# Performance work log

Measured on AMD Instinct MI355X. Metric: run time of the kernel, lower is better.

## Reference

```python
import jax, jax.numpy as jnp
import numpy as np

NUM_HEADS = 16

def setup_inputs() -> dict:
    key = jax.random.key(0)
    ks = jax.random.split(key, 5)
    d_model = 1024
    x = jax.random.normal(ks[0], (2, 2048, d_model), dtype=jnp.float32)
    # xavier-uniform-like scale for square [d_model, d_model] weights
    lim = float(np.sqrt(6.0 / (d_model + d_model)))
    def w(k):
        return jax.random.uniform(k, (d_model, d_model), dtype=jnp.float32, minval=-lim, maxval=lim)
    return {"x": x, "Wq": w(ks[1]), "Wk": w(ks[2]), "Wv": w(ks[3]), "Wo": w(ks[4])}

def reference(x, Wq, Wk, Wv, Wo):
    B, S, D = x.shape
    H = NUM_HEADS
    dk = D // H
    # project: torch does x @ W.T
    def split_heads(t):
        return t.reshape(B, S, H, dk).transpose(0, 2, 1, 3)  # [B,H,S,dk]
    q = split_heads(x @ Wq.T)
    k = split_heads(x @ Wk.T)
    v = split_heads(x @ Wv.T)
    scores = jnp.einsum('bhqd,bhkd->bhqk', q, k) / jnp.sqrt(jnp.float32(dk))
    causal = jnp.tril(jnp.ones((S, S), dtype=bool))  # True where attended
    scores = jnp.where(causal[None, None], scores, -jnp.inf)
    probs = jax.nn.softmax(scores, axis=-1)
    out = jnp.einsum('bhqk,bhkd->bhqd', probs, v)  # [B,H,S,dk]
    out = out.transpose(0, 2, 1, 3).reshape(B, S, D)
    return out @ Wo.T
```

## Files before the change

kernel.cpp:

```cpp
#include <hip/hip_runtime.h>
#include <stdint.h>

#define BATCH  2
#define SEQ    2048
#define DMODEL 1024
#define NHEADS 16
#define DKH    64
#define MTOT   (BATCH*SEQ)
#define VSTR   (SEQ + 32)

typedef unsigned short u16;
typedef __bf16 bf16x8 __attribute__((ext_vector_type(8)));
typedef float  f32x4  __attribute__((ext_vector_type(4)));

extern "C" __device__ float __ocml_native_exp2_f32(float);

__device__ __forceinline__ u16 f2bf(float f) {
  union { float f; uint32_t u; } v; v.f = f;
  uint32_t u = v.u;
  return (u16)((u + 0x7FFFu + ((u >> 16) & 1u)) >> 16);
}
__device__ __forceinline__ float bf2f(u16 h) {
  union { uint32_t u; float f; } v; v.u = (uint32_t)h << 16; return v.f;
}

__device__ __forceinline__ void gld_lds16(const void* g, void* l) {
  __builtin_amdgcn_global_load_lds(
      (__attribute__((address_space(1))) void*)g,
      (__attribute__((address_space(3))) void*)l, 16, 0, 0);
}

__global__ void cvt_f32_bf16(const float* __restrict__ src, u16* __restrict__ dst) {
  size_t i = ((size_t)blockIdx.x * 256 + threadIdx.x) * 4;
  float4 f = *(const float4*)(src + i);
  ushort4 o;
  o.x = f2bf(f.x); o.y = f2bf(f.y); o.z = f2bf(f.z); o.w = f2bf(f.w);
  *(ushort4*)(dst + i) = o;
}
__global__ void cvt_w(const float* __restrict__ a, const float* __restrict__ b,
                      const float* __restrict__ c, const float* __restrict__ d,
                      u16* __restrict__ dst) {
  const float* srcs[4] = {a, b, c, d};
  const float* s = srcs[blockIdx.y];
  size_t i = ((size_t)blockIdx.x * 256 + threadIdx.x) * 4;
  float4 f = *(const float4*)(s + i);
  ushort4 o;
  o.x = f2bf(f.x); o.y = f2bf(f.y); o.z = f2bf(f.z); o.w = f2bf(f.w);
  *(ushort4*)(dst + (size_t)blockIdx.y * (DMODEL*DMODEL) + i) = o;
}

__device__ __forceinline__ void gemm_core64(const u16* A, const u16* W,
                                            int m0, int n0, f32x4 acc[4][2],
                                            u16* lA, u16* lB) {
  const int tid  = threadIdx.x;
  const int lane = tid & 63;
  const int lrow = lane & 15;
  const int quad = lane >> 4;
  const int wave = tid >> 6;
  const int wm   = (wave & 1) * 64;
  const int wn   = (wave >> 1) * 32;
  const int sx   = lrow & 7;

  for (int k0 = 0; k0 < DMODEL; k0 += 64) {
    #pragma unroll
    for (int r = 0; r < 4; ++r) {
      int off  = r * 4096 + tid * 16;
      int row  = off >> 7;
      int c16  = (off >> 4) & 7;
      int colb = (c16 ^ (row & 7)) << 4;
      gld_lds16((const char*)A + ((size_t)(m0 + row) * DMODEL + k0) * 2 + colb,
                (char*)lA + off);
    }
    #pragma unroll
    for (int r = 0; r < 2; ++r) {
      int off  = r * 4096 + tid * 16;
      int row  = off >> 7;
      int c16  = (off >> 4) & 7;
      int colb = (c16 ^ (row & 7)) << 4;
      gld_lds16((const char*)W + ((size_t)(n0 + row) * DMODEL + k0) * 2 + colb,
                (char*)lB + off);
    }
    __syncthreads();
    #pragma unroll
    for (int ks = 0; ks < 2; ++ks) {
      bf16x8 a[4], b[2];
      const int ro = ((((ks << 2) | quad) ^ sx) << 3);
      #pragma unroll
      for (int i = 0; i < 4; ++i)
        a[i] = *(const bf16x8*)(lA + (wm + i*16 + lrow) * 64 + ro);
      #pragma unroll
      for (int j = 0; j < 2; ++j)
        b[j] = *(const bf16x8*)(lB + (wn + j*16 + lrow) * 64 + ro);
      #pragma unroll
      for (int i = 0; i < 4; ++i)
        #pragma unroll
        for (int j = 0; j < 2; ++j)
          acc[i][j] = __builtin_amdgcn_mfma_f32_16x16x32_bf16(a[i], b[j], acc[i][j], 0, 0, 0);
    }
    __syncthreads();
  }
}

__global__ __launch_bounds__(256, 3) void gemm_qkv(
    const u16* __restrict__ xb, const u16* __restrict__ wq,
    const u16* __restrict__ wk, const u16* __restrict__ wv,
    u16* __restrict__ q, u16* __restrict__ k, u16* __restrict__ v, float qscale) {
  __shared__ __align__(16) u16 lA[128 * 64];
  __shared__ __align__(16) u16 lB[64 * 64];
  const int z = blockIdx.z;
  const u16* W = (z == 0) ? wq : (z == 1) ? wk : wv;
  u16* out     = (z == 0) ? q  : (z == 1) ? k  : v;
  const float scale = (z == 0) ? qscale : 1.0f;
  const int m0 = blockIdx.x * 128, n0 = blockIdx.y * 64;
  f32x4 acc[4][2] = {};
  gemm_core64(xb, W, m0, n0, acc, lA, lB);

  const int lane = threadIdx.x & 63;
  const int wave = threadIdx.x >> 6;
  const int wm = (wave & 1) * 64, wn = (wave >> 1) * 32;
  const int rb = (lane >> 4) * 4, cb = lane & 15;
  const int h = n0 >> 6;
  if (z == 2) {
    #pragma unroll
    for (int i = 0; i < 4; ++i)
      #pragma unroll
      for (int j = 0; j < 2; ++j) {
        int row0 = m0 + wm + i*16 + rb;
        int d_   = wn + j*16 + cb;
        int b_ = row0 >> 11, s0 = row0 & 2047;
        ushort4 pk;
        pk.x = f2bf(acc[i][j][0]); pk.y = f2bf(acc[i][j][1]);
        pk.z = f2bf(acc[i][j][2]); pk.w = f2bf(acc[i][j][3]);
        *(ushort4*)&out[((size_t)(b_*NHEADS + h) * DKH + d_) * VSTR + s0] = pk;
      }
  } else {
    #pragma unroll
    for (int i = 0; i < 4; ++i)
      #pragma unroll
      for (int j = 0; j < 2; ++j)
        #pragma unroll
        for (int r = 0; r < 4; ++r) {
          int row = m0 + wm + i*16 + rb + r;
          int d_  = wn + j*16 + cb;
          int b_ = row >> 11, s_ = row & 2047;
          out[(((size_t)(b_*NHEADS + h) * SEQ + s_) << 6) + d_] =
              f2bf(acc[i][j][r] * scale);
        }
  }
}

__global__ __launch_bounds__(256, 3) void gemm_out(
    const u16* __restrict__ ab, const u16* __restrict__ wo, float* __restrict__ out) {
  __shared__ __align__(16) u16 lA[128 * 64];
  __shared__ __align__(16) u16 lB[64 * 64];
  const int m0 = blockIdx.x * 128, n0 = blockIdx.y * 64;
  f32x4 acc[4][2] = {};
  gemm_core64(ab, wo, m0, n0, acc, lA, lB);

  const int lane = threadIdx.x & 63;
  const int wave = threadIdx.x >> 6;
  const int wm = (wave & 1) * 64, wn = (wave >> 1) * 32;
  const int rb = (lane >> 4) * 4, cb = lane & 15;
  #pragma unroll
  for (int i = 0; i < 4; ++i)
    #pragma unroll
    for (int j = 0; j < 2; ++j)
      #pragma unroll
      for (int r = 0; r < 4; ++r)
        out[(size_t)(m0 + wm + i*16 + rb + r) * DMODEL + (n0 + wn + j*16 + cb)]
            = acc[i][j][r];
}

#define PSTR 68
__device__ const uint8_t JT[60] = {
  124,125,120,121,116,117,112,113,108,109,104,105,100,101,96,97,92,93,
  88,84,80,76,72,68,64,60,56,52,48,44,
  89,40, 85,36, 81,32, 126,77,28, 122,73,24, 118,69,20, 114,65,16,
  110,61,12, 106,57,8, 102,53,4, 98,49,0
};

__global__ __launch_bounds__(64, 2) void attn(
    const u16* __restrict__ Q, const u16* __restrict__ K,
    const u16* __restrict__ V, u16* __restrict__ O,
    u16* __restrict__ po, float* __restrict__ pl) {
  __shared__ __align__(16) u16 Ps[4][16 * PSTR];

  const int lane = threadIdx.x & 63;
  const int lrow = lane & 15;
  const int quad = lane >> 4;
  const int kq   = quad * 8;

  const int g  = blockIdx.x >> 5;
  const int bh = blockIdx.x & 31;
  const int e  = JT[g];
  const int p  = e >> 2, c = e & 3;
  const int lo = c * 12;
  const int hi = (p + 1 < lo + 12) ? p + 1 : lo + 12;

  const u16* Qg = Q + (size_t)bh * SEQ * DKH;
  const u16* Kg = K + (size_t)bh * SEQ * DKH;
  const u16* Vg = V + (size_t)bh * DKH * VSTR;

  bf16x8 aq[4][2];
  #pragma unroll
  for (int i = 0; i < 4; ++i)
    #pragma unroll
    for (int ks = 0; ks < 2; ++ks)
      aq[i][ks] = *(const bf16x8*)(Qg + (size_t)(64*p + 16*i + lrow) * DKH + ks*32 + kq);

  f32x4 o_acc[4][4] = {};
  float l_acc[4][4] = {};

  const u16* kbase = Kg + (size_t)lrow * DKH + kq;
  const u16* vbase = Vg + (size_t)lrow * VSTR + kq;

  for (int t = lo; t < hi; ++t) {
    bf16x8 kf[2][4], vf[2][4];
    #pragma unroll
    for (int ks = 0; ks < 2; ++ks)
      #pragma unroll
      for (int j = 0; j < 4; ++j) {
        kf[ks][j] = *(const bf16x8*)(kbase + (size_t)t*64*DKH + j*16*DKH + ks*32);
        vf[ks][j] = *(const bf16x8*)(vbase + t*64 + (size_t)j*16*VSTR + ks*32);
      }
    const bool mk = (t == p);

    #pragma unroll
    for (int i = 0; i < 4; ++i) {
      f32x4 s_acc[4] = {};
      #pragma unroll
      for (int ks = 0; ks < 2; ++ks)
        #pragma unroll
        for (int j = 0; j < 4; ++j)
          s_acc[j] = __builtin_amdgcn_mfma_f32_16x16x32_bf16(aq[i][ks], kf[ks][j], s_acc[j], 0, 0, 0);

      if (mk) {
        const int qloc = 16*i + quad*4;
        #pragma unroll
        for (int j = 0; j < 4; ++j) {
          int kloc = j*16 + lrow;
          #pragma unroll
          for (int r = 0; r < 4; ++r)
            if (kloc > qloc + r) s_acc[j][r] = -1e30f;
        }
      }

      #pragma unroll
      for (int j = 0; j < 4; ++j)
        #pragma unroll
        for (int r = 0; r < 4; ++r) {
          float pv = __ocml_native_exp2_f32(s_acc[j][r]);
          l_acc[i][r] += pv;
          union { float f; uint32_t u; } cv; cv.f = pv;
          Ps[i][(quad*4 + r) * PSTR + j*16 + lrow] = (u16)(cv.u >> 16);
        }

      #pragma unroll
      for (int ks = 0; ks < 2; ++ks) {
        bf16x8 ap = *(const bf16x8*)(&Ps[i][lrow * PSTR + ks*32 + kq]);
        #pragma unroll
        for (int j = 0; j < 4; ++j)
          o_acc[i][j] = __builtin_amdgcn_mfma_f32_16x16x32_bf16(ap, vf[ks][j], o_acc[i][j], 0, 0, 0);
      }
    }
  }

  float lr[4][4];
  #pragma unroll
  for (int i = 0; i < 4; ++i)
    #pragma unroll
    for (int r = 0; r < 4; ++r) {
      float sm = l_acc[i][r];
      #pragma unroll
      for (int d = 1; d < 16; d <<= 1) sm += __shfl_xor(sm, d, 64);
      lr[i][r] = sm;
    }

  if (p <= 11) {
    const int h = bh & 15, b_ = bh >> 4;
    #pragma unroll
    for (int i = 0; i < 4; ++i)
      #pragma unroll
      for (int j = 0; j < 4; ++j)
        #pragma unroll
        for (int r = 0; r < 4; ++r) {
          int sg = 64*p + 16*i + quad*4 + r;
          O[(size_t)(b_ * SEQ + sg) * DMODEL + h * DKH + j*16 + lrow]
              = f2bf(o_acc[i][j][r] / lr[i][r]);
        }
  } else {
    const int base = (p < 24) ? (p - 12) * 2 : 24 + (p - 24) * 3;
    const int slot = (base + c) * 32 + bh;
    #pragma unroll
    for (int i = 0; i < 4; ++i) {
      #pragma unroll
      for (int j = 0; j < 4; ++j) {
        ushort4 pk;
        pk.x = f2bf(o_acc[i][j][0]); pk.y = f2bf(o_acc[i][j][1]);
        pk.z = f2bf(o_acc[i][j][2]); pk.w = f2bf(o_acc[i][j][3]);
        *(ushort4*)&po[(size_t)slot * 4096 + (j*16 + lrow) * 64 + 16*i + quad*4] = pk;
      }
      if (lrow == 0)
        #pragma unroll
        for (int r = 0; r < 4; ++r)
          pl[slot * 64 + 16*i + quad*4 + r] = lr[i][r];
    }
  }
}

__global__ __launch_bounds__(256) void combine(
    const u16* __restrict__ po, const float* __restrict__ pl, u16* __restrict__ ab) {
  __shared__ u16 Ls[64][68];
  const int b  = blockIdx.x;
  const int p  = 12 + (b >> 5);
  const int bh = b & 31;
  const int t  = threadIdx.x;
  const int col = t >> 2;
  const int r0  = (t & 3) * 16;
  const int base = (p < 24) ? (p - 12) * 2 : 24 + (p - 24) * 3;
  const int nc   = (p < 24) ? 2 : 3;

  float acc[16], lsum[16];
  {
    const size_t s0 = (size_t)(base * 32 + bh);
    const u16*   q0 = po + s0 * 4096 + col * 64 + r0;
    const float* l0 = pl + s0 * 64 + r0;
    #pragma unroll
    for (int q4 = 0; q4 < 4; ++q4) {
      ushort4 a = *(const ushort4*)(q0 + q4 * 4);
      ushort4 c2 = *(const ushort4*)(q0 + 32 * 4096 + q4 * 4);
      acc[q4*4+0] = bf2f(a.x) + bf2f(c2.x);
      acc[q4*4+1] = bf2f(a.y) + bf2f(c2.y);
      acc[q4*4+2] = bf2f(a.z) + bf2f(c2.z);
      acc[q4*4+3] = bf2f(a.w) + bf2f(c2.w);
      float4 f = *(const float4*)(l0 + q4 * 4);
      float4 g = *(const float4*)(l0 + 32 * 64 + q4 * 4);
      lsum[q4*4+0] = f.x + g.x; lsum[q4*4+1] = f.y + g.y;
      lsum[q4*4+2] = f.z + g.z; lsum[q4*4+3] = f.w + g.w;
    }
    if (nc == 3) {
      const u16*   q2 = q0 + (size_t)64 * 4096;
      const float* l2 = l0 + (size_t)64 * 64;
      #pragma unroll
      for (int q4 = 0; q4 < 4; ++q4) {
        ushort4 a = *(const ushort4*)(q2 + q4 * 4);
        acc[q4*4+0] += bf2f(a.x); acc[q4*4+1] += bf2f(a.y);
        acc[q4*4+2] += bf2f(a.z); acc[q4*4+3] += bf2f(a.w);
        float4 f = *(const float4*)(l2 + q4 * 4);
        lsum[q4*4+0] += f.x; lsum[q4*4+1] += f.y;
        lsum[q4*4+2] += f.z; lsum[q4*4+3] += f.w;
      }
    }
  }
  #pragma unroll
  for (int q = 0; q < 16; ++q)
    Ls[r0 + q][col] = f2bf(acc[q] / lsum[q]);
  __syncthreads();

  const int row = t >> 2;
  const int c0  = (t & 3) * 16;
  const int b_ = bh >> 4, h = bh & 15;
  u16* dst = ab + (size_t)(b_ * SEQ + 64 * p + row) * DMODEL + h * DKH + c0;
  #pragma unroll
  for (int q = 0; q < 16; q += 4)
    *(ushort4*)(dst + q) = *(const ushort4*)&Ls[row][c0 + q];
}

extern "C" void kernel_launch(void* const* d_in, const int* in_sizes, int n_in,
                              void* d_out, int out_size, void* d_ws, size_t ws_size,
                              hipStream_t stream) {
  const float* x  = (const float*)d_in[0];
  const float* Wq = (const float*)d_in[1];
  const float* Wk = (const float*)d_in[2];
  const float* Wv = (const float*)d_in[3];
  const float* Wo = (const float*)d_in[4];
  float* out = (float*)d_out;

  u16* xb  = (u16*)d_ws;
  u16* wqb = xb  + (size_t)MTOT * DMODEL;
  u16* wkb = wqb + (size_t)DMODEL * DMODEL;
  u16* wvb = wkb + (size_t)DMODEL * DMODEL;
  u16* wob = wvb + (size_t)DMODEL * DMODEL;
  u16* qb  = wob + (size_t)DMODEL * DMODEL;
  u16* kb  = qb  + (size_t)MTOT * DMODEL;
  u16* vb  = kb  + (size_t)MTOT * DMODEL;
  u16* ab  = vb  + (size_t)BATCH * NHEADS * DKH * VSTR;
  u16* po  = xb;
  float* pl = (float*)(po + (size_t)1536 * 4096);

  cvt_f32_bf16<<<MTOT * DMODEL / 1024, 256, 0, stream>>>(x, xb);
  cvt_w<<<dim3(DMODEL * DMODEL / 1024, 4), 256, 0, stream>>>(Wq, Wk, Wv, Wo, wqb);

  const float qscale = 0.125f * 1.44269504088896340736f;
  gemm_qkv<<<dim3(32, 16, 3), 256, 0, stream>>>(
      xb, wqb, wkb, wvb, qb, kb, vb, qscale);

  attn<<<1920, 64, 0, stream>>>(qb, kb, vb, ab, po, pl);
  combine<<<640, 256, 0, stream>>>(po, pl, ab);

  gemm_out<<<dim3(32, 16), 256, 0, stream>>>(ab, wob, out);
}
```

Measured before the change: 176.2 us.

## Fuse QKV projections into one GEMM tile and split attention KV into finer chunks

The QKV GEMM now computes Q, K and V for the same 128x64 tile in one block, loading each x tile into LDS once and reusing it across three weight tiles, instead of launching three separate z-slices. This cuts repeated reads of x and launches a third as many blocks, but each block holds three times the accumulators and more LDS, which may lower occupancy. The causal attention split also changes from 12-block to 8-block KV chunks, giving more work items (2560) and a reworked combine for up to four partials, to balance load better. The partial buffers are moved to a separate workspace region because they no longer fit in the reused xb area.

After: 171.3 us. -2.8%, faster.

```diff
diff --git a/kernel.cpp b/kernel.cpp
--- a/kernel.cpp
+++ b/kernel.cpp
@@ -47,6 +47,108 @@
   ushort4 o;
   o.x = f2bf(f.x); o.y = f2bf(f.y); o.z = f2bf(f.z); o.w = f2bf(f.w);
   *(ushort4*)(dst + (size_t)blockIdx.y * (DMODEL*DMODEL) + i) = o;
+}
+
+__global__ __launch_bounds__(256, 3) void gemm_qkv(
+    const u16* __restrict__ xb, const u16* __restrict__ wq,
+    const u16* __restrict__ wk, const u16* __restrict__ wv,
+    u16* __restrict__ q, u16* __restrict__ k, u16* __restrict__ v, float qscale) {
+  __shared__ __align__(16) u16 lA[128 * 64];
+  __shared__ __align__(16) u16 lB[3][64 * 64];
+
+  const int tid  = threadIdx.x;
+  const int lane = tid & 63;
+  const int lrow = lane & 15;
+  const int quad = lane >> 4;
+  const int wave = tid >> 6;
+  const int wm   = (wave & 1) * 64;
+  const int wn   = (wave >> 1) * 32;
+  const int sx   = lrow & 7;
+  const int m0 = blockIdx.x * 128, n0 = blockIdx.y * 64;
+  const u16* Ws[3] = {wq, wk, wv};
+
+  f32x4 acc[3][4][2] = {};
+
+  for (int k0 = 0; k0 < DMODEL; k0 += 64) {
+    #pragma unroll
+    for (int r = 0; r < 4; ++r) {
+      int off  = r * 4096 + tid * 16;
+      int row  = off >> 7;
+      int c16  = (off >> 4) & 7;
+      int colb = (c16 ^ (row & 7)) << 4;
+      gld_lds16((const char*)xb + ((size_t)(m0 + row) * DMODEL + k0) * 2 + colb,
+                (char*)lA + off);
+    }
+    #pragma unroll
+    for (int z = 0; z < 3; ++z)
+      #pragma unroll
+      for (int r = 0; r < 2; ++r) {
+        int off  = r * 4096 + tid * 16;
+        int row  = off >> 7;
+        int c16  = (off >> 4) & 7;
+        int colb = (c16 ^ (row & 7)) << 4;
+        gld_lds16((const char*)Ws[z] + ((size_t)(n0 + row) * DMODEL + k0) * 2 + colb,
+                  (char*)&lB[z][0] + off);
+      }
+    __syncthreads();
+    #pragma unroll
+    for (int ks = 0; ks < 2; ++ks) {
+      const int ro = ((((ks << 2) | quad) ^ sx) << 3);
+      bf16x8 a[4], b[3][2];
+      #pragma unroll
+      for (int i = 0; i < 4; ++i)
+        a[i] = *(const bf16x8*)(lA + (wm + i*16 + lrow) * 64 + ro);
+      #pragma unroll
+      for (int z = 0; z < 3; ++z)
+        #pragma unroll
+        for (int j = 0; j < 2; ++j)
+          b[z][j] = *(const bf16x8*)(&lB[z][0] + (wn + j*16 + lrow) * 64 + ro);
+      #pragma unroll
+      for (int z = 0; z < 3; ++z)
+        #pragma unroll
+        for (int i = 0; i < 4; ++i)
+          #pragma unroll
+          for (int j = 0; j < 2; ++j)
+            acc[z][i][j] = __builtin_amdgcn_mfma_f32_16x16x32_bf16(a[i], b[z][j], acc[z][i][j], 0, 0, 0);
+    }
+    __syncthreads();
+  }
+
+  const int rb = quad * 4, cb = lrow;
+  const int h  = blockIdx.y;
+  u16* outs[3] = {q, k, v};
+  #pragma unroll
+  for (int z = 0; z < 3; ++z) {
+    u16* out = outs[z];
+    if (z == 2) {
+      #pragma unroll
+      for (int i = 0; i < 4; ++i)
+        #pragma unroll
+        for (int j = 0; j < 2; ++j) {
+          int row0 = m0 + wm + i*16 + rb;
+          int d_   = wn + j*16 + cb;
+          int b_ = row0 >> 11, s0 = row0 & 2047;
+          ushort4 pk;
+          pk.x = f2bf(acc[z][i][j][0]); pk.y = f2bf(acc[z][i][j][1]);
+          pk.z = f2bf(acc[z][i][j][2]); pk.w = f2bf(acc[z][i][j][3]);
+          *(ushort4*)&out[((size_t)(b_*NHEADS + h) * DKH + d_) * VSTR + s0] = pk;
+        }
+    } else {
+      const float scale = (z == 0) ? qscale : 1.0f;
+      #pragma unroll
+      for (int i = 0; i < 4; ++i)
+        #pragma unroll
+        for (int j = 0; j < 2; ++j)
+          #pragma unroll
+          for (int r = 0; r < 4; ++r) {
+            int row = m0 + wm + i*16 + rb + r;
+            int d_  = wn + j*16 + cb;
+            int b_ = row >> 11, s_ = row & 2047;
+            out[(((size_t)(b_*NHEADS + h) * SEQ + s_) << 6) + d_] =
+                f2bf(acc[z][i][j][r] * scale);
+          }
+    }
+  }
 }
 
 __device__ __forceinline__ void gemm_core64(const u16* A, const u16* W,
@@ -101,54 +203,6 @@
   }
 }
 
-__global__ __launch_bounds__(256, 3) void gemm_qkv(
-    const u16* __restrict__ xb, const u16* __restrict__ wq,
-    const u16* __restrict__ wk, const u16* __restrict__ wv,
-    u16* __restrict__ q, u16* __restrict__ k, u16* __restrict__ v, float qscale) {
-  __shared__ __align__(16) u16 lA[128 * 64];
-  __shared__ __align__(16) u16 lB[64 * 64];
-  const int z = blockIdx.z;
-  const u16* W = (z == 0) ? wq : (z == 1) ? wk : wv;
-  u16* out     = (z == 0) ? q  : (z == 1) ? k  : v;
-  const float scale = (z == 0) ? qscale : 1.0f;
-  const int m0 = blockIdx.x * 128, n0 = blockIdx.y * 64;
-  f32x4 acc[4][2] = {};
-  gemm_core64(xb, W, m0, n0, acc, lA, lB);
-
-  const int lane = threadIdx.x & 63;
-  const int wave = threadIdx.x >> 6;
-  const int wm = (wave & 1) * 64, wn = (wave >> 1) * 32;
-  const int rb = (lane >> 4) * 4, cb = lane & 15;
-  const int h = n0 >> 6;
-  if (z == 2) {
-    #pragma unroll
-    for (int i = 0; i < 4; ++i)
-      #pragma unroll
-      for (int j = 0; j < 2; ++j) {
-        int row0 = m0 + wm + i*16 + rb;
-        int d_   = wn + j*16 + cb;
-        int b_ = row0 >> 11, s0 = row0 & 2047;
-        ushort4 pk;
-        pk.x = f2bf(acc[i][j][0]); pk.y = f2bf(acc[i][j][1]);
-        pk.z = f2bf(acc[i][j][2]); pk.w = f2bf(acc[i][j][3]);
-        *(ushort4*)&out[((size_t)(b_*NHEADS + h) * DKH + d_) * VSTR + s0] = pk;
-      }
-  } else {
-    #pragma unroll
-    for (int i = 0; i < 4; ++i)
-      #pragma unroll
-      for (int j = 0; j < 2; ++j)
-        #pragma unroll
-        for (int r = 0; r < 4; ++r) {
-          int row = m0 + wm + i*16 + rb + r;
-          int d_  = wn + j*16 + cb;
-          int b_ = row >> 11, s_ = row & 2047;
-          out[(((size_t)(b_*NHEADS + h) * SEQ + s_) << 6) + d_] =
-              f2bf(acc[i][j][r] * scale);
-        }
-  }
-}
-
 __global__ __launch_bounds__(256, 3) void gemm_out(
     const u16* __restrict__ ab, const u16* __restrict__ wo, float* __restrict__ out) {
   __shared__ __align__(16) u16 lA[128 * 64];
@@ -172,11 +226,12 @@
 }
 
 #define PSTR 68
-__device__ const uint8_t JT[60] = {
-  124,125,120,121,116,117,112,113,108,109,104,105,100,101,96,97,92,93,
-  88,84,80,76,72,68,64,60,56,52,48,44,
-  89,40, 85,36, 81,32, 126,77,28, 122,73,24, 118,69,20, 114,65,16,
-  110,61,12, 106,57,8, 102,53,4, 98,49,0
+__device__ const uint8_t JT[80] = {
+  124,125,126,127, 120,121,122, 116,117,118, 112,113,114, 108,109,110,
+  104,105,106, 100,101,102, 96,97,98, 92,93,94, 88,89, 84,85, 80,81,
+  76,77, 72,73, 68,69, 64,65, 60,61, 56, 52, 48, 44, 40, 36, 32, 28,
+  123,90,57,24, 119,86,53,20, 115,82,49,16, 111,78,45,12,
+  107,74,41,8, 103,70,37,4, 99,66,33,0
 };
 
 __global__ __launch_bounds__(64, 2) void attn(
@@ -194,8 +249,8 @@
   const int bh = blockIdx.x & 31;
   const int e  = JT[g];
   const int p  = e >> 2, c = e & 3;
-  const int lo = c * 12;
-  const int hi = (p + 1 < lo + 12) ? p + 1 : lo + 12;
+  const int lo = c * 8;
+  const int hi = (p + 1 < lo + 8) ? p + 1 : lo + 8;
 
   const u16* Qg = Q + (size_t)bh * SEQ * DKH;
   const u16* Kg = K + (size_t)bh * SEQ * DKH;
@@ -276,7 +331,7 @@
       lr[i][r] = sm;
     }
 
-  if (p <= 11) {
+  if (p <= 7) {
     const int h = bh & 15, b_ = bh >> 4;
     #pragma unroll
     for (int i = 0; i < 4; ++i)
@@ -289,7 +344,9 @@
               = f2bf(o_acc[i][j][r] / lr[i][r]);
         }
   } else {
-    const int base = (p < 24) ? (p - 12) * 2 : 24 + (p - 24) * 3;
+    const int base = (p < 16) ? (p - 8) * 2
+                   : (p < 24) ? 16 + (p - 16) * 3
+                   :            40 + (p - 24) * 4;
     const int slot = (base + c) * 32 + bh;
     #pragma unroll
     for (int i = 0; i < 4; ++i) {
@@ -312,44 +369,53 @@
     const u16* __restrict__ po, const float* __restrict__ pl, u16* __restrict__ ab) {
   __shared__ u16 Ls[64][68];
   const int b  = blockIdx.x;
-  const int p  = 12 + (b >> 5);
+  const int p  = 8 + (b >> 5);
   const int bh = b & 31;
   const int t  = threadIdx.x;
   const int col = t >> 2;
   const int r0  = (t & 3) * 16;
-  const int base = (p < 24) ? (p - 12) * 2 : 24 + (p - 24) * 3;
-  const int nc   = (p < 24) ? 2 : 3;
+  const int base = (p < 16) ? (p - 8) * 2
+                 : (p < 24) ? 16 + (p - 16) * 3
+                 :            40 + (p - 24) * 4;
+  const int nc   = (p < 16) ? 2 : (p < 24) ? 3 : 4;
 
   float acc[16], lsum[16];
-  {
-    const size_t s0 = (size_t)(base * 32 + bh);
-    const u16*   q0 = po + s0 * 4096 + col * 64 + r0;
-    const float* l0 = pl + s0 * 64 + r0;
+  const size_t s0 = (size_t)(base * 32 + bh);
+  const u16*   q0 = po + s0 * 4096 + col * 64 + r0;
+  const float* l0 = pl + s0 * 64 + r0;
+  #pragma unroll
+  for (int q4 = 0; q4 < 4; ++q4) {
+    ushort4 a  = *(const ushort4*)(q0 + q4 * 4);
+    ushort4 c2 = *(const ushort4*)(q0 + (size_t)32 * 4096 + q4 * 4);
+    acc[q4*4+0] = bf2f(a.x) + bf2f(c2.x);
+    acc[q4*4+1] = bf2f(a.y) + bf2f(c2.y);
+    acc[q4*4+2] = bf2f(a.z) + bf2f(c2.z);
+    acc[q4*4+3] = bf2f(a.w) + bf2f(c2.w);
+    float4 f = *(const float4*)(l0 + q4 * 4);
+    float4 g = *(const float4*)(l0 + 32 * 64 + q4 * 4);
+    lsum[q4*4+0] = f.x + g.x; lsum[q4*4+1] = f.y + g.y;
+    lsum[q4*4+2] = f.z + g.z; lsum[q4*4+3] = f.w + g.w;
+  }
+  if (nc >= 3) {
     #pragma unroll
     for (int q4 = 0; q4 < 4; ++q4) {
-      ushort4 a = *(const ushort4*)(q0 + q4 * 4);
-      ushort4 c2 = *(const ushort4*)(q0 + 32 * 4096 + q4 * 4);
-      acc[q4*4+0] = bf2f(a.x) + bf2f(c2.x);
-      acc[q4*4+1] = bf2f(a.y) + bf2f(c2.y);
-      acc[q4*4+2] = bf2f(a.z) + bf2f(c2.z);
-      acc[q4*4+3] = bf2f(a.w) + bf2f(c2.w);
-      float4 f = *(const float4*)(l0 + q4 * 4);
-      float4 g = *(const float4*)(l0 + 32 * 64 + q4 * 4);
-      lsum[q4*4+0] = f.x + g.x; lsum[q4*4+1] = f.y + g.y;
-      lsum[q4*4+2] = f.z + g.z; lsum[q4*4+3] = f.w + g.w;
-    }
-    if (nc == 3) {
-      const u16*   q2 = q0 + (size_t)64 * 4096;
-      const float* l2 = l0 + (size_t)64 * 64;
-      #pragma unroll
-      for (int q4 = 0; q4 < 4; ++q4) {
-        ushort4 a = *(const ushort4*)(q2 + q4 * 4);
-        acc[q4*4+0] += bf2f(a.x); acc[q4*4+1] += bf2f(a.y);
-        acc[q4*4+2] += bf2f(a.z); acc[q4*4+3] += bf2f(a.w);
-        float4 f = *(const float4*)(l2 + q4 * 4);
-        lsum[q4*4+0] += f.x; lsum[q4*4+1] += f.y;
-        lsum[q4*4+2] += f.z; lsum[q4*4+3] += f.w;
-      }
+      ushort4 a = *(const ushort4*)(q0 + (size_t)64 * 4096 + q4 * 4);
+      acc[q4*4+0] += bf2f(a.x); acc[q4*4+1] += bf2f(a.y);
+      acc[q4*4+2] += bf2f(a.z); acc[q4*4+3] += bf2f(a.w);
+      float4 f = *(const float4*)(l0 + 64 * 64 + q4 * 4);
+      lsum[q4*4+0] += f.x; lsum[q4*4+1] += f.y;
+      lsum[q4*4+2] += f.z; lsum[q4*4+3] += f.w;
+    }
+  }
+  if (nc == 4) {
+    #pragma unroll
+    for (int q4 = 0; q4 < 4; ++q4) {
+      ushort4 a = *(const ushort4*)(q0 + (size_t)96 * 4096 + q4 * 4);
+      acc[q4*4+0] += bf2f(a.x); acc[q4*4+1] += bf2f(a.y);
+      acc[q4*4+2] += bf2f(a.z); acc[q4*4+3] += bf2f(a.w);
+      float4 f = *(const float4*)(l0 + 96 * 64 + q4 * 4);
+      lsum[q4*4+0] += f.x; lsum[q4*4+1] += f.y;
+      lsum[q4*4+2] += f.z; lsum[q4*4+3] += f.w;
     }
   }
   #pragma unroll
@@ -385,18 +451,18 @@
   u16* kb  = qb  + (size_t)MTOT * DMODEL;
   u16* vb  = kb  + (size_t)MTOT * DMODEL;
   u16* ab  = vb  + (size_t)BATCH * NHEADS * DKH * VSTR;
-  u16* po  = xb;
-  float* pl = (float*)(po + (size_t)1536 * 4096);
+  u16* po  = ab  + (size_t)MTOT * DMODEL;
+  float* pl = (float*)(po + (size_t)2304 * 4096);
 
   cvt_f32_bf16<<<MTOT * DMODEL / 1024, 256, 0, stream>>>(x, xb);
   cvt_w<<<dim3(DMODEL * DMODEL / 1024, 4), 256, 0, stream>>>(Wq, Wk, Wv, Wo, wqb);
 
   const float qscale = 0.125f * 1.44269504088896340736f;
-  gemm_qkv<<<dim3(32, 16, 3), 256, 0, stream>>>(
+  gemm_qkv<<<dim3(32, 16), 256, 0, stream>>>(
       xb, wqb, wkb, wvb, qb, kb, vb, qscale);
 
-  attn<<<1920, 64, 0, stream>>>(qb, kb, vb, ab, po, pl);
-  combine<<<640, 256, 0, stream>>>(po, pl, ab);
+  attn<<<2560, 64, 0, stream>>>(qb, kb, vb, ab, po, pl);
+  combine<<<768, 256, 0, stream>>>(po, pl, ab);
 
   gemm_out<<<dim3(32, 16), 256, 0, stream>>>(ab, wob, out);
 }
```
